# Optimization experiments

Measured on AMD Instinct MI355X. Metric: run time of the kernel, lower is better.

Reference implementation:

```python
import jax, jax.numpy as jnp
import numpy as np

B, L, H, NH, D, I = 2, 2048, 2048, 16, 128, 8192
EPS = 1e-6
ROPE_BASE = 10000.0


def rms_norm(x, w):
    x32 = x.astype(jnp.float32)
    n = x32 * jax.lax.rsqrt(jnp.mean(x32 * x32, axis=-1, keepdims=True) + EPS)
    return (n * w).astype(x.dtype)


def rope(x, offset):
    # x: [B, L, H, D], non-traditional (half-split) RoPE
    d = x.shape[-1]
    half = d // 2
    inv_freq = 1.0 / (ROPE_BASE ** (jnp.arange(half, dtype=jnp.float32) * 2.0 / d))
    pos = jnp.arange(x.shape[1], dtype=jnp.float32) + offset
    ang = pos[:, None] * inv_freq[None, :]              # [L, half]
    cos = jnp.cos(ang)[None, :, None, :]
    sin = jnp.sin(ang)[None, :, None, :]
    x1, x2 = x[..., :half], x[..., half:]
    out = jnp.concatenate([x1 * cos - x2 * sin, x2 * cos + x1 * sin], axis=-1)
    return out.astype(x.dtype)


def setup_inputs() -> dict:
    key = jax.random.key(0)
    ks = jax.random.split(key, 9)
    s = 0.02
    causal = jnp.where(jnp.tril(jnp.ones((L, L), dtype=bool)), 0.0, -1e9).astype(jnp.float32)
    return {
        "x": jax.random.normal(ks[0], (B, L, H), dtype=jnp.float32),
        "ln1_w": jnp.ones((H,), dtype=jnp.float32),
        "ln2_w": jnp.ones((H,), dtype=jnp.float32),
        "wq": jax.random.normal(ks[1], (H, H), dtype=jnp.float32) * s,
        "wk": jax.random.normal(ks[2], (H, H), dtype=jnp.float32) * s,
        "wv": jax.random.normal(ks[3], (H, H), dtype=jnp.float32) * s,
        "wo": jax.random.normal(ks[4], (H, H), dtype=jnp.float32) * s,
        "w_gate": jax.random.normal(ks[5], (I, H), dtype=jnp.float32) * s,
        "w_up": jax.random.normal(ks[6], (I, H), dtype=jnp.float32) * s,
        "w_down": jax.random.normal(ks[7], (H, I), dtype=jnp.float32) * s,
        "mask": causal,
        "offset": 0,
    }


def reference(x, ln1_w, ln2_w, wq, wk, wv, wo, w_gate, w_up, w_down, mask, offset):
    residual = x
    h = rms_norm(x, ln1_w)
    # QKV projections (torch Linear: y = x @ W.T)
    q = jnp.einsum("ble,oe->blo", h, wq).reshape(B, L, NH, D)
    k = jnp.einsum("ble,oe->blo", h, wk).reshape(B, L, NH, D)
    v = jnp.einsum("ble,oe->blo", h, wv).reshape(B, L, NH, D)
    q = rope(q, offset)
    k = rope(k, offset)
    # [B, NH, L, D]
    q = q.transpose(0, 2, 1, 3)
    k = k.transpose(0, 2, 1, 3)
    v = v.transpose(0, 2, 1, 3)
    scores = jnp.einsum("bhqd,bhkd->bhqk", q.astype(jnp.float32), k.astype(jnp.float32))
    scores = scores / np.sqrt(D).astype(np.float32)
    if mask is not None:
        scores = scores + mask
    probs = jax.nn.softmax(scores, axis=-1).astype(v.dtype)
    attn = jnp.einsum("bhqk,bhkd->bhqd", probs, v)
    attn = attn.transpose(0, 2, 1, 3).reshape(B, L, NH * D)
    h = jnp.einsum("blo,eo->ble", attn, wo)
    x = h + residual
    residual = x
    h = rms_norm(x, ln2_w)
    gate = jax.nn.silu(jnp.einsum("ble,ie->bli", h, w_gate))
    up = jnp.einsum("ble,ie->bli", h, w_up)
    mlp = jnp.einsum("bli,ei->ble", gate * up, w_down)
    return mlp + residual
```

## Files before the change

### kernel.cpp

```cpp
#include <hip/hip_runtime.h>
#include <stdint.h>

#define B_ 2
#define L_ 2048
#define H_ 2048
#define NH_ 16
#define D_ 128
#define I_ 8192
#define M_ (B_*L_)

typedef unsigned short u16;
typedef __attribute__((ext_vector_type(8))) short bf16x8;
typedef __attribute__((ext_vector_type(4))) float f32x4;

__device__ __forceinline__ u16 f2bf(float f) {
  union { float f; uint32_t u; } c; c.f = f;
  return (u16)((c.u + 0x7fffu + ((c.u >> 16) & 1u)) >> 16);
}
__device__ __forceinline__ float bf2f(u16 h) {
  union { uint32_t u; float f; } c; c.u = ((uint32_t)h) << 16;
  return c.f;
}
__device__ __forceinline__ void gload16(const void* g, void* l) {
  __builtin_amdgcn_global_load_lds(
      (__attribute__((address_space(1))) void*)g,
      (__attribute__((address_space(3))) void*)l, 16, 0, 0);
}

__global__ void cvt_w(const float* __restrict__ src, u16* __restrict__ dst, int n4) {
  int i = blockIdx.x * blockDim.x + threadIdx.x;
  if (i >= n4) return;
  float4 v = ((const float4*)src)[i];
  ushort4 o;
  o.x = f2bf(v.x); o.y = f2bf(v.y); o.z = f2bf(v.z); o.w = f2bf(v.w);
  ((ushort4*)dst)[i] = o;
}

__global__ __launch_bounds__(256) void down_reduce(const u16* __restrict__ p0,
                                                   const u16* __restrict__ p1,
                                                   const float* __restrict__ res,
                                                   float* __restrict__ out, int n4) {
  int i = blockIdx.x * blockDim.x + threadIdx.x;
  if (i >= n4) return;
  ushort4 a = ((const ushort4*)p0)[i];
  ushort4 b = ((const ushort4*)p1)[i];
  float4 r = ((const float4*)res)[i];
  float4 o;
  o.x = bf2f(a.x) + bf2f(b.x) + r.x;
  o.y = bf2f(a.y) + bf2f(b.y) + r.y;
  o.z = bf2f(a.z) + bf2f(b.z) + r.z;
  o.w = bf2f(a.w) + bf2f(b.w) + r.w;
  ((float4*)out)[i] = o;
}

__global__ __launch_bounds__(256) void rmsnorm_k(const float* __restrict__ x,
                                                 const float* __restrict__ w,
                                                 u16* __restrict__ out) {
  int row = blockIdx.x;
  int t = threadIdx.x;
  const float4* xr = (const float4*)(x + (size_t)row * H_);
  float4 a = xr[t * 2], b = xr[t * 2 + 1];
  float s = a.x*a.x + a.y*a.y + a.z*a.z + a.w*a.w
          + b.x*b.x + b.y*b.y + b.z*b.z + b.w*b.w;
  for (int m = 1; m < 64; m <<= 1) s += __shfl_xor(s, m);
  __shared__ float sm[4];
  if ((t & 63) == 0) sm[t >> 6] = s;
  __syncthreads();
  float tot = sm[0] + sm[1] + sm[2] + sm[3];
  float rs = rsqrtf(tot / (float)H_ + 1e-6f);
  const float4* wr = (const float4*)w;
  float4 w0 = wr[t * 2], w1 = wr[t * 2 + 1];
  ushort4 o0, o1;
  o0.x = f2bf(a.x * rs * w0.x); o0.y = f2bf(a.y * rs * w0.y);
  o0.z = f2bf(a.z * rs * w0.z); o0.w = f2bf(a.w * rs * w0.w);
  o1.x = f2bf(b.x * rs * w1.x); o1.y = f2bf(b.y * rs * w1.y);
  o1.z = f2bf(b.z * rs * w1.z); o1.w = f2bf(b.w * rs * w1.w);
  ushort4* orow = (ushort4*)(out + (size_t)row * H_);
  orow[t * 2] = o0; orow[t * 2 + 1] = o1;
}

__global__ void rope_tab(float* __restrict__ cosT, float* __restrict__ sinT,
                         const int* __restrict__ offp) {
  int i = blockIdx.x * blockDim.x + threadIdx.x;
  int d = i & 63, l = i >> 6;
  float inv = powf(10000.0f, -(float)d / 64.0f);
  float ang = (float)(l + *offp) * inv;
  cosT[i] = cosf(ang);
  sinT[i] = sinf(ang);
}

__global__ void rope_apply(u16* __restrict__ qk, const float* __restrict__ cosT,
                           const float* __restrict__ sinT) {
  int i = blockIdx.x * blockDim.x + threadIdx.x;
  int d = i & 63;
  size_t row = (size_t)(i >> 6);
  int l = (int)(row & (L_ - 1));
  u16* p = qk + row * D_;
  float x1 = bf2f(p[d]), x2 = bf2f(p[d + 64]);
  float c = cosT[l * 64 + d], s = sinT[l * 64 + d];
  p[d]      = f2bf(x1 * c - x2 * s);
  p[d + 64] = f2bf(x2 * c + x1 * s);
}

__global__ __launch_bounds__(256) void vtrans_k(const u16* __restrict__ v,
                                                u16* __restrict__ vt) {
  __shared__ u16 tile[64][65];
  int l0 = blockIdx.x * 64, d0 = blockIdx.y * 64;
  size_t base = (size_t)blockIdx.z * L_ * D_;
  int t = threadIdx.x;
  int tr = t >> 3, tc = (t & 7) * 8;
  #pragma unroll
  for (int it = 0; it < 2; ++it) {
    int r = tr + it * 32;
    const u16* src = v + base + (size_t)(l0 + r) * D_ + d0 + tc;
    ushort4 u0 = ((const ushort4*)src)[0], u1 = ((const ushort4*)src)[1];
    tile[r][tc + 0] = u0.x; tile[r][tc + 1] = u0.y;
    tile[r][tc + 2] = u0.z; tile[r][tc + 3] = u0.w;
    tile[r][tc + 4] = u1.x; tile[r][tc + 5] = u1.y;
    tile[r][tc + 6] = u1.z; tile[r][tc + 7] = u1.w;
  }
  __syncthreads();
  #pragma unroll
  for (int it = 0; it < 2; ++it) {
    int r = tr + it * 32;
    u16* dst = vt + base + (size_t)(d0 + r) * L_ + l0 + tc;
    ushort4 o0, o1;
    o0.x = tile[tc + 0][r]; o0.y = tile[tc + 1][r];
    o0.z = tile[tc + 2][r]; o0.w = tile[tc + 3][r];
    o1.x = tile[tc + 4][r]; o1.y = tile[tc + 5][r];
    o1.z = tile[tc + 6][r]; o1.w = tile[tc + 7][r];
    ((ushort4*)dst)[0] = o0; ((ushort4*)dst)[1] = o1;
  }
}

#define EPI_QKV 0
#define EPI_SILU 1
#define EPI_MUL 2
#define EPI_ADDRES 3
#define EPI_PART 4
#define EPI_QKV3 5

template <int EPI>
__global__ __launch_bounds__(256)
void gemm_bt(const u16* __restrict__ A, const u16* __restrict__ Bw,
             int M, int N, int K,
             u16* outb, float* outf, const float* __restrict__ resf) {
  __shared__ __attribute__((aligned(16))) u16 At[128 * 64];
  __shared__ __attribute__((aligned(16))) u16 Bt[128 * 64];
  int tid = threadIdx.x;
  int w = tid >> 6, lane = tid & 63;
  int r16 = lane & 15, g4 = lane >> 4;
  int wr = w >> 1, wc = w & 1;
  int m0 = blockIdx.y * 128;
  int n0 = blockIdx.x * 128;
  f32x4 acc[4][4] = {};
  const char* Ab = (const char*)A;
  const char* Bb = (const char*)Bw;
  int nk = K >> 6;
  for (int kt = 0; kt < nk; ++kt) {
    int k0 = kt << 6;
    #pragma unroll
    for (int i = 0; i < 4; ++i) {
      int uoff = i * 4096 + w * 1024;
      int lin = uoff + lane * 16;
      int row = lin >> 7;
      int colB = lin & 127;
      gload16(Ab + ((size_t)(m0 + row) * K + k0) * 2 + colB, (char*)At + uoff);
      gload16(Bb + ((size_t)(n0 + row) * K + k0) * 2 + colB, (char*)Bt + uoff);
    }
    __syncthreads();
    #pragma unroll
    for (int kk = 0; kk < 2; ++kk) {
      bf16x8 af[4], bfr[4];
      #pragma unroll
      for (int m = 0; m < 4; ++m)
        af[m] = *(const bf16x8*)&At[(wr * 64 + m * 16 + r16) * 64 + kk * 32 + g4 * 8];
      #pragma unroll
      for (int n = 0; n < 4; ++n)
        bfr[n] = *(const bf16x8*)&Bt[(wc * 64 + n * 16 + r16) * 64 + kk * 32 + g4 * 8];
      #pragma unroll
      for (int m = 0; m < 4; ++m)
        #pragma unroll
        for (int n = 0; n < 4; ++n)
          acc[m][n] = __builtin_amdgcn_mfma_f32_16x16x32_bf16(af[m], bfr[n], acc[m][n], 0, 0, 0);
    }
    __syncthreads();
  }
  #pragma unroll
  for (int m = 0; m < 4; ++m) {
    #pragma unroll
    for (int n = 0; n < 4; ++n) {
      #pragma unroll
      for (int r = 0; r < 4; ++r) {
        int row = m0 + wr * 64 + m * 16 + g4 * 4 + r;
        int col = n0 + wc * 64 + n * 16 + r16;
        float val = acc[m][n][r];
        if (EPI == EPI_QKV) {
          int b = row >> 11, l = row & 2047;
          int hh = col >> 7, d = col & 127;
          outb[((((size_t)b * NH_ + hh) * L_ + l) << 7) + d] = f2bf(val);
        } else if (EPI == EPI_SILU) {
          float sg = val / (1.0f + __expf(-val));
          outb[(size_t)row * N + col] = f2bf(sg);
        } else if (EPI == EPI_MUL) {
          float g = bf2f(outb[(size_t)row * N + col]);
          outb[(size_t)row * N + col] = f2bf(g * val);
        } else {
          outf[(size_t)row * N + col] = val + resf[(size_t)row * N + col];
        }
      }
    }
  }
}

template <int EPI>
__global__ __launch_bounds__(512, 2)
void gemm256(const u16* __restrict__ A, const u16* __restrict__ Bw,
             int M, int N, int K, int nk,
             u16* __restrict__ outb, u16* __restrict__ outb2) {
  __shared__ __attribute__((aligned(16))) u16 Asm[2][2][8192];
  __shared__ __attribute__((aligned(16))) u16 Bsm[2][2][8192];
  int tid = threadIdx.x;
  int wid = tid >> 6, lane = tid & 63;
  int r16 = lane & 15, g4 = lane >> 4;
  int nwg = gridDim.x, bid = blockIdx.x;
  int q8 = nwg >> 3, r8 = nwg & 7, xcd = bid & 7, loc = bid >> 3;
  int wgall = (xcd < r8 ? xcd * (q8 + 1) : r8 * (q8 + 1) + (xcd - r8) * q8) + loc;
  int nwg_geo = (M >> 8) * (N >> 8);
  int ks = wgall / nwg_geo;
  int wg = wgall % nwg_geo;
  int MX = M >> 8;
  int m0 = (wg % MX) * 256;
  int n0 = (wg / MX) * 256;
  const char* Ab = (const char*)(A + (size_t)ks * nk * 64);
  const char* Bb = (const char*)(Bw + (size_t)ks * nk * 64);
  u16* ob = (EPI == EPI_PART && ks) ? outb2 : outb;

  f32x4 acc[2][2][4][2] = {};
  bf16x8 afr[4][2];
  bf16x8 bfr[2][2][2];

  auto STAGE = [&](int kt1, int sel) {
    if (kt1 >= nk) return;
    int buf = kt1 & 1;
    int k0 = kt1 << 6;
    const char* gb; char* lb; int row0;
    if (sel == 0)      { gb = Ab; row0 = m0;       lb = (char*)&Asm[buf][0][0]; }
    else if (sel == 3) { gb = Ab; row0 = m0 + 128; lb = (char*)&Asm[buf][1][0]; }
    else if (sel == 1) { gb = Bb; row0 = n0;       lb = (char*)&Bsm[buf][0][0]; }
    else               { gb = Bb; row0 = n0 + 128; lb = (char*)&Bsm[buf][1][0]; }
    #pragma unroll
    for (int j = 0; j < 2; ++j) {
      int p = j * 8192 + wid * 1024 + lane * 16;
      int r = p >> 7;
      int cb = (p & 127) ^ ((r & 7) << 4);
      gload16(gb + ((size_t)(row0 + r) * K + k0) * 2 + cb,
              lb + j * 8192 + wid * 1024);
    }
  };

  STAGE(0, 0); STAGE(0, 1); STAGE(0, 2); STAGE(0, 3);

  const int QM[4] = {0, 0, 1, 1};
  const int QN[4] = {0, 1, 1, 0};

  for (int kt = 0; kt < nk; ++kt) {
    int cur = kt & 1;
    #pragma unroll
    for (int ph = 0; ph < 4; ++ph) {
      if (ph < 3) {
        __builtin_amdgcn_sched_barrier(0);
        asm volatile("s_waitcnt vmcnt(4)" ::: "memory");
      }
      __builtin_amdgcn_s_barrier();
      __builtin_amdgcn_sched_barrier(0);
      const int qm = QM[ph], qn = QN[ph];
      if (ph == 0 || ph == 2) {
        const char* Ah = (const char*)&Asm[cur][qm][0];
        #pragma unroll
        for (int mf = 0; mf < 4; ++mf) {
          int R = (wid >> 2) * 64 + mf * 16 + r16;
          int sw = (R & 7) << 4;
          afr[mf][0] = *(const bf16x8*)(Ah + R * 128 + ((g4 * 16) ^ sw));
          afr[mf][1] = *(const bf16x8*)(Ah + R * 128 + ((64 + g4 * 16) ^ sw));
        }
      }
      if (ph == 0 || ph == 1) {
        const char* Bh = (const char*)&Bsm[cur][qn][0];
        #pragma unroll
        for (int nf = 0; nf < 2; ++nf) {
          int R = (wid & 3) * 32 + nf * 16 + r16;
          int sw = (R & 7) << 4;
          bfr[qn][nf][0] = *(const bf16x8*)(Bh + R * 128 + ((g4 * 16) ^ sw));
          bfr[qn][nf][1] = *(const bf16x8*)(Bh + R * 128 + ((64 + g4 * 16) ^ sw));
        }
      }
      STAGE(kt + 1, ph);
      __builtin_amdgcn_s_setprio(1);
      #pragma unroll
      for (int mf = 0; mf < 4; ++mf)
        #pragma unroll
        for (int nf = 0; nf < 2; ++nf)
          #pragma unroll
          for (int kk = 0; kk < 2; ++kk)
            acc[qm][qn][mf][nf] = __builtin_amdgcn_mfma_f32_16x16x32_bf16(
                afr[mf][kk], bfr[qn][nf][kk], acc[qm][qn][mf][nf], 0, 0, 0);
      __builtin_amdgcn_s_setprio(0);
    }
  }
  #pragma unroll
  for (int qm = 0; qm < 2; ++qm)
    #pragma unroll
    for (int qn = 0; qn < 2; ++qn)
      #pragma unroll
      for (int mf = 0; mf < 4; ++mf)
        #pragma unroll
        for (int nf = 0; nf < 2; ++nf)
          #pragma unroll
          for (int rr = 0; rr < 4; ++rr) {
            int row = m0 + qm * 128 + (wid >> 2) * 64 + mf * 16 + g4 * 4 + rr;
            int col = n0 + qn * 128 + (wid & 3) * 32 + nf * 16 + r16;
            float val = acc[qm][qn][mf][nf][rr];
            if (EPI == EPI_SILU) {
              ob[(size_t)row * N + col] = f2bf(val / (1.0f + __expf(-val)));
            } else if (EPI == EPI_MUL) {
              float g = bf2f(ob[(size_t)row * N + col]);
              ob[(size_t)row * N + col] = f2bf(g * val);
            } else if (EPI == EPI_PART) {
              ob[(size_t)row * N + col] = f2bf(val);
            } else if (EPI == EPI_QKV3) {
              int which = col >> 11, within = col & 2047;
              int hh = within >> 7, d = within & 127;
              int bb = row >> 11, l = row & 2047;
              ob[(size_t)which * M_ * H_ +
                 ((((size_t)bb * NH_ + hh) * L_ + l) << 7) + d] = f2bf(val);
            }
          }
}

__global__ __launch_bounds__(256)
void flash_attn(const u16* __restrict__ q, const u16* __restrict__ k,
                const u16* __restrict__ vt, u16* __restrict__ out) {
  __shared__ __attribute__((aligned(16))) u16 Kt[64 * 128];
  __shared__ __attribute__((aligned(16))) u16 Vt[128 * 64];
  __shared__ __attribute__((aligned(16))) u16 Pl[4][16 * 64];
  int tid = threadIdx.x, w = tid >> 6, lane = tid & 63;
  int r16 = lane & 15, g4 = lane >> 4;
  int b = blockIdx.z, h = blockIdx.y;
  int qt = gridDim.x - 1 - blockIdx.x;
  int q0 = qt * 64;
  size_t bh = (size_t)b * NH_ + h;
  const char* qb = (const char*)(q + bh * L_ * D_);
  const char* kb = (const char*)(k + bh * L_ * D_);
  const char* vb = (const char*)(vt + bh * D_ * L_);
  int qrow = q0 + w * 16 + r16;
  bf16x8 qf[4];
  #pragma unroll
  for (int c = 0; c < 4; ++c)
    qf[c] = *(const bf16x8*)(qb + ((size_t)qrow * 128 + c * 32 + g4 * 8) * 2);
  f32x4 oacc[8] = {};
  float mrow[4], lsum[4];
  #pragma unroll
  for (int r = 0; r < 4; ++r) { mrow[r] = -3.0e38f; lsum[r] = 0.f; }
  int myq = q0 + w * 16 + g4 * 4;
  int ntiles = qt + 1;
  int rsw = (r16 & 7) << 4;
  const float sc = 0.08838834764831845f;
  for (int t = 0; t < ntiles; ++t) {
    int kv0 = t * 64;
    #pragma unroll
    for (int i = 0; i < 4; ++i) {
      int uoff = i * 4096 + w * 1024;
      int lin = uoff + lane * 16;
      int krow = lin >> 8;
      int kcol = (lin & 255) ^ ((krow & 7) << 4);
      gload16(kb + (size_t)(kv0 + krow) * 256 + kcol, (char*)Kt + uoff);
      int vrow = lin >> 7;
      int vcol = (lin & 127) ^ ((vrow & 7) << 4);
      gload16(vb + (size_t)vrow * (L_ * 2) + kv0 * 2 + vcol, (char*)Vt + uoff);
    }
    __syncthreads();
    f32x4 s[4] = {};
    __builtin_amdgcn_s_setprio(1);
    #pragma unroll
    for (int c = 0; c < 4; ++c) {
      #pragma unroll
      for (int n = 0; n < 4; ++n) {
        const char* kp = (const char*)Kt + (n * 16 + r16) * 256
                       + ((c * 64 + g4 * 16) ^ rsw);
        bf16x8 kf = *(const bf16x8*)kp;
        s[n] = __builtin_amdgcn_mfma_f32_16x16x32_bf16(qf[c], kf, s[n], 0, 0, 0);
      }
    }
    __builtin_amdgcn_s_setprio(0);
    #pragma unroll
    for (int r = 0; r < 4; ++r) {
      float rm = -3.0e38f;
      #pragma unroll
      for (int n = 0; n < 4; ++n) {
        float v = s[n][r] * sc;
        int kvi = kv0 + n * 16 + r16;
        if (kvi > myq + r) v = -3.0e38f;
        s[n][r] = v;
        rm = fmaxf(rm, v);
      }
      rm = fmaxf(rm, __shfl_xor(rm, 1));
      rm = fmaxf(rm, __shfl_xor(rm, 2));
      rm = fmaxf(rm, __shfl_xor(rm, 4));
      rm = fmaxf(rm, __shfl_xor(rm, 8));
      float mnew = fmaxf(mrow[r], rm);
      float alpha = __expf(mrow[r] - mnew);
      mrow[r] = mnew;
      lsum[r] *= alpha;
      #pragma unroll
      for (int nf = 0; nf < 8; ++nf) oacc[nf][r] *= alpha;
      int prow = g4 * 4 + r;
      int psw = (prow & 7) << 3;
      #pragma unroll
      for (int n = 0; n < 4; ++n) {
        float pv = __expf(s[n][r] - mnew);
        lsum[r] += pv;
        Pl[w][prow * 64 + ((n * 16 + r16) ^ psw)] = f2bf(pv);
      }
    }
    asm volatile("s_waitcnt lgkmcnt(0)" ::: "memory");
    __builtin_amdgcn_sched_barrier(0);
    __builtin_amdgcn_s_setprio(1);
    #pragma unroll
    for (int kc = 0; kc < 2; ++kc) {
      const char* pp = (const char*)&Pl[w][0] + r16 * 128
                     + ((kc * 64 + g4 * 16) ^ rsw);
      bf16x8 pf = *(const bf16x8*)pp;
      #pragma unroll
      for (int nf = 0; nf < 8; ++nf) {
        const char* vp = (const char*)Vt + (nf * 16 + r16) * 128
                       + ((kc * 64 + g4 * 16) ^ rsw);
        bf16x8 vf = *(const bf16x8*)vp;
        oacc[nf] = __builtin_amdgcn_mfma_f32_16x16x32_bf16(pf, vf, oacc[nf], 0, 0, 0);
      }
    }
    __builtin_amdgcn_s_setprio(0);
    __syncthreads();
  }
  #pragma unroll
  for (int r = 0; r < 4; ++r) {
    float l = lsum[r];
    l += __shfl_xor(l, 1); l += __shfl_xor(l, 2);
    l += __shfl_xor(l, 4); l += __shfl_xor(l, 8);
    float inv = 1.0f / l;
    size_t orow = ((size_t)b * L_ + (myq + r)) * H_ + h * D_;
    #pragma unroll
    for (int nf = 0; nf < 8; ++nf)
      out[orow + nf * 16 + r16] = f2bf(oacc[nf][r] * inv);
  }
}

extern "C" void kernel_launch(void* const* d_in, const int* in_sizes, int n_in,
                              void* d_out, int out_size, void* d_ws, size_t ws_size,
                              hipStream_t stream) {
  (void)in_sizes; (void)n_in; (void)out_size; (void)ws_size;
  const float* x    = (const float*)d_in[0];
  const float* ln1w = (const float*)d_in[1];
  const float* ln2w = (const float*)d_in[2];
  const float* wq   = (const float*)d_in[3];
  const float* wk   = (const float*)d_in[4];
  const float* wv   = (const float*)d_in[5];
  const float* wo   = (const float*)d_in[6];
  const float* wg   = (const float*)d_in[7];
  const float* wu   = (const float*)d_in[8];
  const float* wd   = (const float*)d_in[9];
  const int*   offp = (const int*)d_in[11];
  float* out = (float*)d_out;

  char* p = (char*)d_ws;
  auto alloc = [&](size_t bytes) {
    char* r = p;
    p += (bytes + 255) & ~(size_t)255;
    return r;
  };
  const size_t HH = (size_t)H_ * H_, IH = (size_t)I_ * H_;
  u16* wbuf = (u16*)alloc(IH * 2);
  u16* h1   = (u16*)alloc((size_t)M_ * H_ * 2);
  u16* qb   = (u16*)alloc((size_t)M_ * H_ * 2);
  u16* kb   = (u16*)alloc((size_t)M_ * H_ * 2);
  u16* vb   = (u16*)alloc((size_t)M_ * H_ * 2);
  u16* vtb  = (u16*)alloc((size_t)M_ * H_ * 2);
  u16* attn = (u16*)alloc((size_t)M_ * H_ * 2);
  float* x2 = (float*)alloc((size_t)M_ * H_ * 4);
  float* cosT = (float*)alloc((size_t)L_ * 64 * 4);
  float* sinT = (float*)alloc((size_t)L_ * 64 * 4);
  (void)kb; (void)vb;
  u16* h2    = h1;
  u16* gateb = qb;

  const int nHH4 = (int)(HH / 4), nIH4 = (int)(IH / 4);

  rmsnorm_k<<<M_, 256, 0, stream>>>(x, ln1w, h1);
  rope_tab<<<(L_ * 64) / 256, 256, 0, stream>>>(cosT, sinT, offp);

  cvt_w<<<nHH4 / 256, 256, 0, stream>>>(wq, wbuf, nHH4);
  cvt_w<<<nHH4 / 256, 256, 0, stream>>>(wk, wbuf + HH, nHH4);
  cvt_w<<<nHH4 / 256, 256, 0, stream>>>(wv, wbuf + 2 * HH, nHH4);
  int nwg_qkv = (M_ / 256) * (3 * H_ / 256);
  gemm256<EPI_QKV3><<<nwg_qkv, 512, 0, stream>>>(h1, wbuf, M_, 3 * H_, H_,
                                                 H_ / 64, qb, nullptr);

  int nrope = B_ * NH_ * L_ * 64;
  rope_apply<<<nrope / 256, 256, 0, stream>>>(qb, cosT, sinT);
  rope_apply<<<nrope / 256, 256, 0, stream>>>(qb + (size_t)M_ * H_, cosT, sinT);
  vtrans_k<<<dim3(L_ / 64, D_ / 64, B_ * NH_), 256, 0, stream>>>(
      qb + 2 * (size_t)M_ * H_, vtb);

  flash_attn<<<dim3(L_ / 64, NH_, B_), 256, 0, stream>>>(
      qb, qb + (size_t)M_ * H_, vtb, attn);

  dim3 g1(H_ / 128, M_ / 128);
  cvt_w<<<nHH4 / 256, 256, 0, stream>>>(wo, wbuf, nHH4);
  gemm_bt<EPI_ADDRES><<<g1, 256, 0, stream>>>(attn, wbuf, M_, H_, H_, nullptr, x2, x);
  rmsnorm_k<<<M_, 256, 0, stream>>>(x2, ln2w, h2);

  int nwg256 = (M_ / 256) * (I_ / 256);
  cvt_w<<<nIH4 / 256, 256, 0, stream>>>(wg, wbuf, nIH4);
  gemm256<EPI_SILU><<<nwg256, 512, 0, stream>>>(h2, wbuf, M_, I_, H_,
                                                H_ / 64, gateb, nullptr);
  cvt_w<<<nIH4 / 256, 256, 0, stream>>>(wu, wbuf, nIH4);
  gemm256<EPI_MUL><<<nwg256, 512, 0, stream>>>(h2, wbuf, M_, I_, H_,
                                               H_ / 64, gateb, nullptr);

  cvt_w<<<nIH4 / 256, 256, 0, stream>>>(wd, wbuf, nIH4);
  int nwg_dn = 2 * (M_ / 256) * (H_ / 256);
  gemm256<EPI_PART><<<nwg_dn, 512, 0, stream>>>(gateb, wbuf, M_, H_, I_,
                                                I_ / 128, h1, attn);
  down_reduce<<<(M_ * H_ / 4) / 256, 256, 0, stream>>>(h1, attn, x2, out,
                                                       M_ * H_ / 4);
}
```

Baseline: 859.7 us.

## Double-buffer K/V tiles in flash attention; route Wo projection through split-K gemm256

The flash attention kernel now keeps two LDS buffers each for K and V and issues the global-to-LDS loads for tile t+1 before computing tile t. This is meant to overlap memory latency with MFMA work. It roughly doubles the kernel's LDS footprint, which may lower occupancy. The output projection drops the 128x128 gemm_bt kernel in favour of the larger 256-tile gemm256 with 2-way split-K. Its bf16 partials go to scratch buffers, and an extra down_reduce pass adds them with the residual, which costs some precision and an additional pass over memory.

Measured after the change: 852.4 us (median of 2 runs). No clear change (-0.8%).

```diff
diff --git a/kernel.cpp b/kernel.cpp
--- a/kernel.cpp
+++ b/kernel.cpp
@@ -133,85 +133,10 @@
   }
 }
 
-#define EPI_QKV 0
 #define EPI_SILU 1
 #define EPI_MUL 2
-#define EPI_ADDRES 3
 #define EPI_PART 4
 #define EPI_QKV3 5
-
-template <int EPI>
-__global__ __launch_bounds__(256)
-void gemm_bt(const u16* __restrict__ A, const u16* __restrict__ Bw,
-             int M, int N, int K,
-             u16* outb, float* outf, const float* __restrict__ resf) {
-  __shared__ __attribute__((aligned(16))) u16 At[128 * 64];
-  __shared__ __attribute__((aligned(16))) u16 Bt[128 * 64];
-  int tid = threadIdx.x;
-  int w = tid >> 6, lane = tid & 63;
-  int r16 = lane & 15, g4 = lane >> 4;
-  int wr = w >> 1, wc = w & 1;
-  int m0 = blockIdx.y * 128;
-  int n0 = blockIdx.x * 128;
-  f32x4 acc[4][4] = {};
-  const char* Ab = (const char*)A;
-  const char* Bb = (const char*)Bw;
-  int nk = K >> 6;
-  for (int kt = 0; kt < nk; ++kt) {
-    int k0 = kt << 6;
-    #pragma unroll
-    for (int i = 0; i < 4; ++i) {
-      int uoff = i * 4096 + w * 1024;
-      int lin = uoff + lane * 16;
-      int row = lin >> 7;
-      int colB = lin & 127;
-      gload16(Ab + ((size_t)(m0 + row) * K + k0) * 2 + colB, (char*)At + uoff);
-      gload16(Bb + ((size_t)(n0 + row) * K + k0) * 2 + colB, (char*)Bt + uoff);
-    }
-    __syncthreads();
-    #pragma unroll
-    for (int kk = 0; kk < 2; ++kk) {
-      bf16x8 af[4], bfr[4];
-      #pragma unroll
-      for (int m = 0; m < 4; ++m)
-        af[m] = *(const bf16x8*)&At[(wr * 64 + m * 16 + r16) * 64 + kk * 32 + g4 * 8];
-      #pragma unroll
-      for (int n = 0; n < 4; ++n)
-        bfr[n] = *(const bf16x8*)&Bt[(wc * 64 + n * 16 + r16) * 64 + kk * 32 + g4 * 8];
-      #pragma unroll
-      for (int m = 0; m < 4; ++m)
-        #pragma unroll
-        for (int n = 0; n < 4; ++n)
-          acc[m][n] = __builtin_amdgcn_mfma_f32_16x16x32_bf16(af[m], bfr[n], acc[m][n], 0, 0, 0);
-    }
-    __syncthreads();
-  }
-  #pragma unroll
-  for (int m = 0; m < 4; ++m) {
-    #pragma unroll
-    for (int n = 0; n < 4; ++n) {
-      #pragma unroll
-      for (int r = 0; r < 4; ++r) {
-        int row = m0 + wr * 64 + m * 16 + g4 * 4 + r;
-        int col = n0 + wc * 64 + n * 16 + r16;
-        float val = acc[m][n][r];
-        if (EPI == EPI_QKV) {
-          int b = row >> 11, l = row & 2047;
-          int hh = col >> 7, d = col & 127;
-          outb[((((size_t)b * NH_ + hh) * L_ + l) << 7) + d] = f2bf(val);
-        } else if (EPI == EPI_SILU) {
-          float sg = val / (1.0f + __expf(-val));
-          outb[(size_t)row * N + col] = f2bf(sg);
-        } else if (EPI == EPI_MUL) {
-          float g = bf2f(outb[(size_t)row * N + col]);
-          outb[(size_t)row * N + col] = f2bf(g * val);
-        } else {
-          outf[(size_t)row * N + col] = val + resf[(size_t)row * N + col];
-        }
-      }
-    }
-  }
-}
 
 template <int EPI>
 __global__ __launch_bounds__(512, 2)
@@ -341,8 +266,8 @@
 __global__ __launch_bounds__(256)
 void flash_attn(const u16* __restrict__ q, const u16* __restrict__ k,
                 const u16* __restrict__ vt, u16* __restrict__ out) {
-  __shared__ __attribute__((aligned(16))) u16 Kt[64 * 128];
-  __shared__ __attribute__((aligned(16))) u16 Vt[128 * 64];
+  __shared__ __attribute__((aligned(16))) u16 Kt[2][64 * 128];
+  __shared__ __attribute__((aligned(16))) u16 Vt[2][128 * 64];
   __shared__ __attribute__((aligned(16))) u16 Pl[4][16 * 64];
   int tid = threadIdx.x, w = tid >> 6, lane = tid & 63;
   int r16 = lane & 15, g4 = lane >> 4;
@@ -366,7 +291,9 @@
   int ntiles = qt + 1;
   int rsw = (r16 & 7) << 4;
   const float sc = 0.08838834764831845f;
-  for (int t = 0; t < ntiles; ++t) {
+
+  auto STAGEKV = [&](int t, int buf) {
+    if (t >= ntiles) return;
     int kv0 = t * 64;
     #pragma unroll
     for (int i = 0; i < 4; ++i) {
@@ -374,21 +301,32 @@
       int lin = uoff + lane * 16;
       int krow = lin >> 8;
       int kcol = (lin & 255) ^ ((krow & 7) << 4);
-      gload16(kb + (size_t)(kv0 + krow) * 256 + kcol, (char*)Kt + uoff);
+      gload16(kb + (size_t)(kv0 + krow) * 256 + kcol,
+              (char*)&Kt[buf][0] + uoff);
       int vrow = lin >> 7;
       int vcol = (lin & 127) ^ ((vrow & 7) << 4);
-      gload16(vb + (size_t)vrow * (L_ * 2) + kv0 * 2 + vcol, (char*)Vt + uoff);
-    }
-    __syncthreads();
+      gload16(vb + (size_t)vrow * (L_ * 2) + kv0 * 2 + vcol,
+              (char*)&Vt[buf][0] + uoff);
+    }
+  };
+
+  STAGEKV(0, 0);
+  __syncthreads();
+
+  for (int t = 0; t < ntiles; ++t) {
+    int buf = t & 1;
+    int kv0 = t * 64;
+    STAGEKV(t + 1, buf ^ 1);
+    const char* Kb = (const char*)&Kt[buf][0];
+    const char* Vb = (const char*)&Vt[buf][0];
     f32x4 s[4] = {};
     __builtin_amdgcn_s_setprio(1);
     #pragma unroll
     for (int c = 0; c < 4; ++c) {
       #pragma unroll
       for (int n = 0; n < 4; ++n) {
-        const char* kp = (const char*)Kt + (n * 16 + r16) * 256
-                       + ((c * 64 + g4 * 16) ^ rsw);
-        bf16x8 kf = *(const bf16x8*)kp;
+        bf16x8 kf = *(const bf16x8*)(Kb + (n * 16 + r16) * 256
+                                     + ((c * 64 + g4 * 16) ^ rsw));
         s[n] = __builtin_amdgcn_mfma_f32_16x16x32_bf16(qf[c], kf, s[n], 0, 0, 0);
       }
     }
@@ -428,14 +366,12 @@
     __builtin_amdgcn_s_setprio(1);
     #pragma unroll
     for (int kc = 0; kc < 2; ++kc) {
-      const char* pp = (const char*)&Pl[w][0] + r16 * 128
-                     + ((kc * 64 + g4 * 16) ^ rsw);
-      bf16x8 pf = *(const bf16x8*)pp;
+      bf16x8 pf = *(const bf16x8*)((const char*)&Pl[w][0] + r16 * 128
+                                   + ((kc * 64 + g4 * 16) ^ rsw));
       #pragma unroll
       for (int nf = 0; nf < 8; ++nf) {
-        const char* vp = (const char*)Vt + (nf * 16 + r16) * 128
-                       + ((kc * 64 + g4 * 16) ^ rsw);
-        bf16x8 vf = *(const bf16x8*)vp;
+        bf16x8 vf = *(const bf16x8*)(Vb + (nf * 16 + r16) * 128
+                                     + ((kc * 64 + g4 * 16) ^ rsw));
         oacc[nf] = __builtin_amdgcn_mfma_f32_16x16x32_bf16(pf, vf, oacc[nf], 0, 0, 0);
       }
     }
@@ -489,7 +425,6 @@
   float* x2 = (float*)alloc((size_t)M_ * H_ * 4);
   float* cosT = (float*)alloc((size_t)L_ * 64 * 4);
   float* sinT = (float*)alloc((size_t)L_ * 64 * 4);
-  (void)kb; (void)vb;
   u16* h2    = h1;
   u16* gateb = qb;
 
@@ -514,9 +449,12 @@
   flash_attn<<<dim3(L_ / 64, NH_, B_), 256, 0, stream>>>(
       qb, qb + (size_t)M_ * H_, vtb, attn);
 
-  dim3 g1(H_ / 128, M_ / 128);
   cvt_w<<<nHH4 / 256, 256, 0, stream>>>(wo, wbuf, nHH4);
-  gemm_bt<EPI_ADDRES><<<g1, 256, 0, stream>>>(attn, wbuf, M_, H_, H_, nullptr, x2, x);
+  int nwg_wo = 2 * (M_ / 256) * (H_ / 256);
+  gemm256<EPI_PART><<<nwg_wo, 512, 0, stream>>>(attn, wbuf, M_, H_, H_,
+                                                H_ / 128, kb, vb);
+  down_reduce<<<(M_ * H_ / 4) / 256, 256, 0, stream>>>(kb, vb, x, x2,
+                                                       M_ * H_ / 4);
   rmsnorm_k<<<M_, 256, 0, stream>>>(x2, ln2w, h2);
 
   int nwg256 = (M_ / 256) * (I_ / 256);
```
